# Kernel tuning notes

Hardware: AMD Instinct MI355X
Metric: run time of the kernel (lower is better)

## Reference

```python
import jax, jax.numpy as jnp
import numpy as np

NUM_HEADS = 16


def setup_inputs() -> dict:
    key = jax.random.key(0)
    k1, k2, k3 = jax.random.split(key, 3)
    T, B, E = 2048, 2, 1024
    x = jax.random.normal(k1, (T, B, E), dtype=jnp.float32)
    in_proj_w = jax.random.normal(k2, (E, 3 * E), dtype=jnp.float32) * (E ** -0.5)
    in_proj_b = jnp.zeros((3 * E,), dtype=jnp.float32)
    out_w = jax.random.normal(k3, (E, E), dtype=jnp.float32) * (E ** -0.5)
    out_b = jnp.zeros((E,), dtype=jnp.float32)
    return {"x": x, "in_proj_w": in_proj_w, "in_proj_b": in_proj_b,
            "out_w": out_w, "out_b": out_b}


def reference(x, in_proj_w, in_proj_b, out_w, out_b):
    # x: (tgt_len, bsz, embed_dim) -- seq-first, self-attention (q is k is v)
    T, B, E = x.shape
    H = NUM_HEADS
    D = E // H
    scaling = D ** -0.5
    # packed in-projection: einsum('bne,ef->bnf') over (T,B,E)
    proj = jnp.einsum('tbe,ef->tbf', x, in_proj_w) + in_proj_b
    q, k, v = jnp.split(proj, 3, axis=-1)  # each (T, B, E)
    # reshape to (T, B*H, D) then transpose to (B*H, T, D)
    q = q.reshape(T, B * H, D).transpose(1, 0, 2)
    k = k.reshape(T, B * H, D).transpose(1, 0, 2)
    v = v.reshape(T, B * H, D).transpose(1, 0, 2)
    # full O(T^2) attention matrix, scaling applied after QK^T as in source
    attn = jnp.einsum('bie,bje->bij', q, k) * scaling  # (B*H, T, T)
    attn = jax.nn.softmax(attn, axis=-1)
    out = jnp.einsum('bij,bje->bie', attn, v)  # (B*H, T, D)
    # faithful to source: reshape directly (no head transpose-back)
    out = out.reshape(B, T, E)
    out = jnp.einsum('bte,ef->btf', out, out_w) + out_b
    return out
```

## Files before the change

### kernel.cpp

```cpp
#include <hip/hip_runtime.h>
#include <stdint.h>

#define TSEQ 2048
#define NB 2
#define EMB 1024
#define NHEAD 16
#define HDIM 64
#define KSPLIT 4
#define NT (TSEQ / KSPLIT / 64)
#define QSCALE 0.18033688f

typedef __bf16 bf16x8 __attribute__((ext_vector_type(8)));
typedef __bf16 bf16x4 __attribute__((ext_vector_type(4)));
typedef float f32x4 __attribute__((ext_vector_type(4)));
typedef float f32x16 __attribute__((ext_vector_type(16)));
typedef unsigned int u32x4 __attribute__((ext_vector_type(4)));

__device__ __forceinline__ void gload_lds16(const void* g, void* lds) {
    __builtin_amdgcn_global_load_lds(
        (const __attribute__((address_space(1))) unsigned int*)g,
        (__attribute__((address_space(3))) unsigned int*)lds, 16, 0, 0);
}

__device__ __forceinline__ float fast_exp2(float x) {
#if __has_builtin(__builtin_amdgcn_exp2f)
    return __builtin_amdgcn_exp2f(x);
#else
    return exp2f(x);
#endif
}

__device__ __forceinline__ unsigned cvt_pk_bf16(float lo, float hi) {
    unsigned r;
    asm("v_cvt_pk_bf16_f32 %0, %1, %2" : "=v"(r) : "v"(lo), "v"(hi));
    return r;
}

__device__ __forceinline__ void swap32(unsigned& a, unsigned& b) {
    asm("v_permlane32_swap_b32 %0, %1" : "+v"(a), "+v"(b));
}

__device__ __forceinline__ bf16x8 as_bf16x8(u32x4 u) {
    union { u32x4 u; bf16x8 h; } c;
    c.u = u;
    return c.h;
}

__global__ __launch_bounds__(256) void cvt_x_kernel(
    const float* __restrict__ x, __bf16* __restrict__ xb)
{
    const size_t idx = ((size_t)blockIdx.x * 256 + threadIdx.x) * 4;
    float4 v = *(const float4*)(x + idx);
    bf16x4 o = { (__bf16)v.x, (__bf16)v.y, (__bf16)v.z, (__bf16)v.w };
    *(bf16x4*)(xb + idx) = o;
}

__global__ __launch_bounds__(256) void transpose_cvt_kernel(
    const float* __restrict__ w_in, const float* __restrict__ w_out,
    __bf16* __restrict__ wiT, __bf16* __restrict__ whT)
{
    __shared__ float tile[32][33];
    int bx = blockIdx.x;
    const int by = blockIdx.y;
    const float* src; __bf16* dst; int sn;
    if (bx < 96) { src = w_in;  dst = wiT; sn = 3072; }
    else         { bx -= 96; src = w_out; dst = whT; sn = 1024; }
    const int tx = threadIdx.x, ty = threadIdx.y;
    #pragma unroll
    for (int i = 0; i < 4; ++i)
        tile[ty + i * 8][tx] = src[(size_t)(by * 32 + ty + i * 8) * sn + bx * 32 + tx];
    __syncthreads();
    #pragma unroll
    for (int i = 0; i < 4; ++i) {
        float v = tile[tx][ty + i * 8];
        dst[(size_t)(bx * 32 + ty + i * 8) * 1024 + by * 32 + tx] = (__bf16)v;
    }
}

__global__ __launch_bounds__(256) void gemm_qkv_kernel(
    const __bf16* __restrict__ A, const __bf16* __restrict__ BT,
    const float* __restrict__ bias,
    __bf16* __restrict__ Oq, __bf16* __restrict__ Ok, __bf16* __restrict__ Ov)
{
    __shared__ __align__(16) __bf16 As[128 * 64];
    __shared__ __align__(16) __bf16 Bs[128 * 64];
    const int tid = threadIdx.x;
    const int wave = tid >> 6, lane = tid & 63;
    const int l16 = lane & 15, quad = lane >> 4;
    const int wm = wave >> 1, wn = wave & 1;
    const int m0 = blockIdx.y * 128, n0 = blockIdx.x * 128;

    f32x4 acc[4][4];
    #pragma unroll
    for (int mt = 0; mt < 4; ++mt)
        #pragma unroll
        for (int nt = 0; nt < 4; ++nt)
            #pragma unroll
            for (int r = 0; r < 4; ++r) acc[mt][nt][r] = 0.f;

    int smrow[4], schunk[4], sbase[4];
    #pragma unroll
    for (int i = 0; i < 4; ++i) {
        int linear = (wave * 4 + i) * 64 + lane;
        smrow[i] = linear >> 3;
        schunk[i] = (linear & 7) ^ (smrow[i] & 7);
        sbase[i] = (wave * 4 + i) * 512;
    }

    for (int k0 = 0; k0 < 1024; k0 += 64) {
        #pragma unroll
        for (int i = 0; i < 4; ++i) {
            gload_lds16(A + (size_t)(m0 + smrow[i]) * 1024 + k0 + schunk[i] * 8,
                        As + sbase[i]);
            gload_lds16(BT + (size_t)(n0 + smrow[i]) * 1024 + k0 + schunk[i] * 8,
                        Bs + sbase[i]);
        }
        __syncthreads();
        #pragma unroll
        for (int kk = 0; kk < 2; ++kk) {
            bf16x8 am[4], bn[4];
            #pragma unroll
            for (int mt = 0; mt < 4; ++mt) {
                int row = wm * 64 + mt * 16 + l16;
                int c = (kk * 4 + quad) ^ (row & 7);
                am[mt] = *(const bf16x8*)(As + row * 64 + c * 8);
            }
            #pragma unroll
            for (int nt = 0; nt < 4; ++nt) {
                int row = wn * 64 + nt * 16 + l16;
                int c = (kk * 4 + quad) ^ (row & 7);
                bn[nt] = *(const bf16x8*)(Bs + row * 64 + c * 8);
            }
            #pragma unroll
            for (int mt = 0; mt < 4; ++mt)
                #pragma unroll
                for (int nt = 0; nt < 4; ++nt)
                    acc[mt][nt] = __builtin_amdgcn_mfma_f32_16x16x32_bf16(
                        am[mt], bn[nt], acc[mt][nt], 0, 0, 0);
        }
        __syncthreads();
    }

    #pragma unroll
    for (int nt = 0; nt < 4; ++nt) {
        const int col = n0 + wn * 64 + nt * 16 + l16;
        const float bv = bias[col];
        const int sec = col >> 10, f = col & 1023;
        const int h = f >> 6, d = f & 63;
        #pragma unroll
        for (int mt = 0; mt < 4; ++mt)
            #pragma unroll
            for (int r = 0; r < 4; ++r) {
                const int row = m0 + wm * 64 + mt * 16 + quad * 4 + r;
                float v = acc[mt][nt][r] + bv;
                const int t = row >> 1, b = row & 1;
                const int bh = b * NHEAD + h;
                const size_t idx = ((size_t)bh * TSEQ + t) * HDIM + d;
                if (sec == 0)
                    Oq[idx] = (__bf16)(v * QSCALE);
                else if (sec == 1)
                    Ok[idx] = (__bf16)v;
                else
                    Ov[idx] = (__bf16)v;
            }
    }
}

__global__ __launch_bounds__(256) void vtrans_kernel(
    const __bf16* __restrict__ V, __bf16* __restrict__ Vt)
{
    __shared__ __bf16 T[64 * 67];
    const int bh = blockIdx.y;
    const int t0 = blockIdx.x * 64;
    const int tid = threadIdx.x;
    const int r = tid >> 2;
    const int c = (tid & 3) * 16;
    const __bf16* src = V + ((size_t)bh * TSEQ + t0 + r) * HDIM + c;
    bf16x8 a = *(const bf16x8*)src;
    bf16x8 b = *(const bf16x8*)(src + 8);
    #pragma unroll
    for (int j = 0; j < 8; ++j) {
        T[r * 67 + c + j] = a[j];
        T[r * 67 + c + 8 + j] = b[j];
    }
    __syncthreads();
    const int dr = tid >> 2;
    const int tc = (tid & 3) * 16;
    bf16x8 o0, o1;
    #pragma unroll
    for (int j = 0; j < 8; ++j) {
        o0[j] = T[(tc + j) * 67 + dr];
        o1[j] = T[(tc + 8 + j) * 67 + dr];
    }
    __bf16* dst = Vt + ((size_t)bh * HDIM + dr) * TSEQ + t0 + tc;
    *(bf16x8*)dst = o0;
    *(bf16x8*)(dst + 8) = o1;
}

__global__ __launch_bounds__(256, 4) void attn_mfma_kernel(
    const __bf16* __restrict__ Q, const __bf16* __restrict__ K,
    const __bf16* __restrict__ Vt,
    __bf16* __restrict__ O0, __bf16* __restrict__ O1,
    __bf16* __restrict__ O2, __bf16* __restrict__ O3,
    float* __restrict__ L0, float* __restrict__ L1,
    float* __restrict__ L2, float* __restrict__ L3)
{
    __shared__ __align__(16) __bf16 Ks[2][64 * 64];
    __shared__ __align__(16) __bf16 Vs[2][64 * 64];

    const int tid  = threadIdx.x;
    const int wave = tid >> 6;
    const int lane = tid & 63;
    const int l31  = lane & 31;
    const int hi   = lane >> 5;
    const int m7   = l31 & 7;

    const int lid = blockIdx.x;
    const int xcd = lid & 7;
    const int j   = lid >> 3;
    const int grp = xcd * 16 + (j >> 4);
    const int qb  = j & 15;
    const int bh  = grp >> 2;
    const int z   = grp & 3;

    const int q0   = qb * 128 + wave * 32;
    const int kbase0 = z * (TSEQ / KSPLIT);

    __bf16* __restrict__ Opart = (z == 0) ? O0 : (z == 1) ? O1 : (z == 2) ? O2 : O3;
    float*  __restrict__ Lpart = (z == 0) ? L0 : (z == 1) ? L1 : (z == 2) ? L2 : L3;

    bf16x8 qf[4];
    {
        const __bf16* Qrow = Q + ((size_t)bh * TSEQ + q0 + l31) * HDIM + 8 * hi;
        #pragma unroll
        for (int c = 0; c < 4; ++c)
            qf[c] = *(const bf16x8*)(Qrow + 16 * c);
    }

    f32x16 Oacc[2];
    #pragma unroll
    for (int dt = 0; dt < 2; ++dt)
        #pragma unroll
        for (int r = 0; r < 16; ++r) Oacc[dt][r] = 0.f;
    float l4[4] = {0.f, 0.f, 0.f, 0.f};

    const __bf16* Kbase = K + ((size_t)bh * TSEQ + kbase0) * HDIM;
    const __bf16* Vbase = Vt + (size_t)bh * HDIM * TSEQ + kbase0;

    int srow[2], schk[2];
    #pragma unroll
    for (int i = 0; i < 2; ++i) {
        const int s = wave * 2 + i;
        srow[i] = s * 8 + (lane >> 3);
        schk[i] = (lane & 7) ^ (srow[i] & 7);
    }

#define STAGE(buf, kt)                                                        \
    {                                                                         \
        _Pragma("unroll")                                                     \
        for (int i = 0; i < 2; ++i) {                                         \
            const int s = wave * 2 + i;                                       \
            gload_lds16(Kbase + (size_t)((kt) * 64 + srow[i]) * HDIM          \
                            + schk[i] * 8,                                    \
                        &Ks[buf][s * 512]);                                   \
            gload_lds16(Vbase + (size_t)srow[i] * TSEQ + (kt) * 64            \
                            + schk[i] * 8,                                    \
                        &Vs[buf][s * 512]);                                   \
        }                                                                     \
    }

    STAGE(0, 0);

    for (int kt = 0; kt < NT; ++kt) {
        const int b = kt & 1;
        __syncthreads();
        if (kt + 1 < NT) STAGE(b ^ 1, kt + 1);

        u32x4 pa[4];
        #pragma unroll
        for (int s = 0; s < 2; ++s) {
            f32x16 sacc;
            #pragma unroll
            for (int r = 0; r < 16; ++r) sacc[r] = 0.f;
            #pragma unroll
            for (int c = 0; c < 4; ++c) {
                bf16x8 kf = *(const bf16x8*)(
                    &Ks[b][(32 * s + l31) * 64 + (((c << 1) | hi) ^ m7) * 8]);
                sacc = __builtin_amdgcn_mfma_f32_32x32x16_bf16(
                    kf, qf[c], sacc, 0, 0, 0);
            }
            float p[16];
            #pragma unroll
            for (int r = 0; r < 16; ++r) {
                p[r] = fast_exp2(sacc[r]);
                l4[r & 3] += p[r];
            }
            unsigned x[8];
            #pragma unroll
            for (int i = 0; i < 8; ++i)
                x[i] = cvt_pk_bf16(p[2 * i], p[2 * i + 1]);
            swap32(x[0], x[2]); swap32(x[1], x[3]);
            swap32(x[4], x[6]); swap32(x[5], x[7]);
            pa[2 * s][0] = x[0]; pa[2 * s][1] = x[1];
            pa[2 * s][2] = x[2]; pa[2 * s][3] = x[3];
            pa[2 * s + 1][0] = x[4]; pa[2 * s + 1][1] = x[5];
            pa[2 * s + 1][2] = x[6]; pa[2 * s + 1][3] = x[7];
        }

        #pragma unroll
        for (int dt = 0; dt < 2; ++dt)
            #pragma unroll
            for (int ks = 0; ks < 4; ++ks) {
                bf16x8 vf = *(const bf16x8*)(
                    &Vs[b][(dt * 32 + l31) * 64 + (((ks << 1) | hi) ^ m7) * 8]);
                Oacc[dt] = __builtin_amdgcn_mfma_f32_32x32x16_bf16(
                    as_bf16x8(pa[ks]), vf, Oacc[dt], 0, 0, 0);
            }
    }
#undef STAGE

    {
        float v = (l4[0] + l4[1]) + (l4[2] + l4[3]);
        v += __shfl_xor(v, 32);
        if (hi == 0)
            Lpart[(size_t)bh * TSEQ + q0 + l31] = v;
    }

    const size_t base = ((size_t)bh * TSEQ + q0) * HDIM;
    #pragma unroll
    for (int dt = 0; dt < 2; ++dt)
        #pragma unroll
        for (int r = 0; r < 16; ++r) {
            const int q = (r & 3) + 8 * (r >> 2) + 4 * hi;
            Opart[base + (size_t)q * HDIM + dt * 32 + l31] =
                (__bf16)Oacc[dt][r];
        }
}

__global__ __launch_bounds__(256) void normalize_kernel(
    const __bf16* __restrict__ O0, const __bf16* __restrict__ O1,
    const __bf16* __restrict__ O2, const __bf16* __restrict__ O3,
    const float* __restrict__ L0, const float* __restrict__ L1,
    const float* __restrict__ L2, const float* __restrict__ L3,
    __bf16* __restrict__ Ob)
{
    const size_t gid = (size_t)blockIdx.x * 256 + threadIdx.x;
    const size_t idx = gid * 8;
    const size_t qi = idx >> 6;
    const float inv = 1.f / (L0[qi] + L1[qi] + L2[qi] + L3[qi]);
    bf16x8 a = *(const bf16x8*)(O0 + idx);
    bf16x8 b = *(const bf16x8*)(O1 + idx);
    bf16x8 c = *(const bf16x8*)(O2 + idx);
    bf16x8 d = *(const bf16x8*)(O3 + idx);
    bf16x8 o;
    #pragma unroll
    for (int j = 0; j < 8; ++j)
        o[j] = (__bf16)((((float)a[j] + (float)b[j]) +
                         ((float)c[j] + (float)d[j])) * inv);
    *(bf16x8*)(Ob + idx) = o;
}

__global__ __launch_bounds__(256) void gemm_out_kernel(
    const __bf16* __restrict__ A, const __bf16* __restrict__ BT,
    const float* __restrict__ bias, float* __restrict__ out)
{
    __shared__ __align__(16) __bf16 As[64 * 64];
    __shared__ __align__(16) __bf16 Bs[64 * 64];
    const int tid = threadIdx.x;
    const int wave = tid >> 6, lane = tid & 63;
    const int l16 = lane & 15, quad = lane >> 4;
    const int wm = wave >> 1, wn = wave & 1;
    const int m0 = blockIdx.y * 64, n0 = blockIdx.x * 64;

    f32x4 acc[2][2];
    #pragma unroll
    for (int mt = 0; mt < 2; ++mt)
        #pragma unroll
        for (int nt = 0; nt < 2; ++nt)
            #pragma unroll
            for (int r = 0; r < 4; ++r) acc[mt][nt][r] = 0.f;

    int srow[2], schk[2], sbase[2];
    #pragma unroll
    for (int i = 0; i < 2; ++i) {
        const int s = wave * 2 + i;
        srow[i] = s * 8 + (lane >> 3);
        schk[i] = (lane & 7) ^ (srow[i] & 7);
        sbase[i] = s * 512;
    }

    for (int k0 = 0; k0 < 1024; k0 += 64) {
        #pragma unroll
        for (int i = 0; i < 2; ++i) {
            gload_lds16(A + (size_t)(m0 + srow[i]) * 1024 + k0 + schk[i] * 8,
                        As + sbase[i]);
            gload_lds16(BT + (size_t)(n0 + srow[i]) * 1024 + k0 + schk[i] * 8,
                        Bs + sbase[i]);
        }
        __syncthreads();
        #pragma unroll
        for (int kk = 0; kk < 2; ++kk) {
            bf16x8 am[2], bn[2];
            #pragma unroll
            for (int mt = 0; mt < 2; ++mt) {
                int row = wm * 32 + mt * 16 + l16;
                int c = (kk * 4 + quad) ^ (row & 7);
                am[mt] = *(const bf16x8*)(As + row * 64 + c * 8);
            }
            #pragma unroll
            for (int nt = 0; nt < 2; ++nt) {
                int row = wn * 32 + nt * 16 + l16;
                int c = (kk * 4 + quad) ^ (row & 7);
                bn[nt] = *(const bf16x8*)(Bs + row * 64 + c * 8);
            }
            #pragma unroll
            for (int mt = 0; mt < 2; ++mt)
                #pragma unroll
                for (int nt = 0; nt < 2; ++nt)
                    acc[mt][nt] = __builtin_amdgcn_mfma_f32_16x16x32_bf16(
                        am[mt], bn[nt], acc[mt][nt], 0, 0, 0);
        }
        __syncthreads();
    }

    #pragma unroll
    for (int nt = 0; nt < 2; ++nt) {
        const int col = n0 + wn * 32 + nt * 16 + l16;
        const float bv = bias[col];
        #pragma unroll
        for (int mt = 0; mt < 2; ++mt)
            #pragma unroll
            for (int r = 0; r < 4; ++r) {
                const int row = m0 + wm * 32 + mt * 16 + quad * 4 + r;
                out[(size_t)row * 1024 + col] = acc[mt][nt][r] + bv;
            }
    }
}

extern "C" void kernel_launch(void* const* d_in, const int* in_sizes, int n_in,
                              void* d_out, int out_size, void* d_ws, size_t ws_size,
                              hipStream_t stream) {
    const float* x     = (const float*)d_in[0];
    const float* w_in  = (const float*)d_in[1];
    const float* b_in  = (const float*)d_in[2];
    const float* w_out = (const float*)d_in[3];
    const float* b_out = (const float*)d_in[4];
    float* out = (float*)d_out;

    const size_t M1 = (size_t)1024 * 1024;
    __bf16* ws  = (__bf16*)d_ws;
    __bf16* xb  = ws;
    __bf16* wiT = xb  + 4 * M1;
    __bf16* whT = wiT + 3 * M1;
    __bf16* Qb  = whT + 1 * M1;
    __bf16* Kb  = Qb  + 4 * M1;
    __bf16* Vt  = Kb  + 4 * M1;
    __bf16* O0  = Vt  + 4 * M1;
    __bf16* O1  = O0  + 4 * M1;
    float*  L0  = (float*)(O1 + 4 * M1);
    float*  L1  = L0 + 65536;
    float*  L2  = L1 + 65536;
    float*  L3  = L2 + 65536;
    __bf16* Vb  = (__bf16*)d_out;
    __bf16* O2  = (__bf16*)d_out;
    __bf16* O3  = O2 + 4 * M1;
    __bf16* Ob  = xb;

    cvt_x_kernel<<<4096, 256, 0, stream>>>(x, xb);
    transpose_cvt_kernel<<<dim3(128, 32), dim3(32, 8), 0, stream>>>(
        w_in, w_out, wiT, whT);
    gemm_qkv_kernel<<<dim3(24, 32), 256, 0, stream>>>(
        xb, wiT, b_in, Qb, Kb, Vb);
    vtrans_kernel<<<dim3(32, 32), 256, 0, stream>>>(Vb, Vt);
    attn_mfma_kernel<<<dim3(2048), 256, 0, stream>>>(
        Qb, Kb, Vt, O0, O1, O2, O3, L0, L1, L2, L3);
    normalize_kernel<<<2048, 256, 0, stream>>>(
        O0, O1, O2, O3, L0, L1, L2, L3, Ob);
    gemm_out_kernel<<<dim3(16, 64), 256, 0, stream>>>(
        Ob, whT, b_out, out);
}
```

Before: 199.2 us.

## Merge prep kernels, double query rows per attention wave, enlarge out-GEMM tiles

Three separate changes. The x conversion and weight transpose kernels become one launch, removing a launch. Each attention wave now handles 64 query rows in two groups that share each K/V fragment read from LDS, so the grid halves and occupancy is lowered to 2 blocks per CU. The output GEMM moves from 64x64 to 128x128 tiles with 4x4 MFMA accumulators per wave, raising reuse per loaded tile. The cost is higher register pressure and fewer blocks, which could reduce latency hiding.

```diff
diff --git a/kernel.cpp b/kernel.cpp
--- a/kernel.cpp
+++ b/kernel.cpp
@@ -46,26 +46,28 @@
     return c.h;
 }
 
-__global__ __launch_bounds__(256) void cvt_x_kernel(
-    const float* __restrict__ x, __bf16* __restrict__ xb)
-{
-    const size_t idx = ((size_t)blockIdx.x * 256 + threadIdx.x) * 4;
-    float4 v = *(const float4*)(x + idx);
-    bf16x4 o = { (__bf16)v.x, (__bf16)v.y, (__bf16)v.z, (__bf16)v.w };
-    *(bf16x4*)(xb + idx) = o;
-}
-
-__global__ __launch_bounds__(256) void transpose_cvt_kernel(
-    const float* __restrict__ w_in, const float* __restrict__ w_out,
-    __bf16* __restrict__ wiT, __bf16* __restrict__ whT)
+__global__ __launch_bounds__(256) void prep_kernel(
+    const float* __restrict__ x, const float* __restrict__ w_in,
+    const float* __restrict__ w_out,
+    __bf16* __restrict__ xb, __bf16* __restrict__ wiT, __bf16* __restrict__ whT)
 {
     __shared__ float tile[32][33];
-    int bx = blockIdx.x;
-    const int by = blockIdx.y;
+    int bid = blockIdx.x;
+    const int tid = threadIdx.x;
+    if (bid < 4096) {
+        const size_t idx = ((size_t)bid * 256 + tid) * 4;
+        float4 v = *(const float4*)(x + idx);
+        bf16x4 o = { (__bf16)v.x, (__bf16)v.y, (__bf16)v.z, (__bf16)v.w };
+        *(bf16x4*)(xb + idx) = o;
+        return;
+    }
+    bid -= 4096;
+    int bx = bid & 127;
+    const int by = bid >> 7;
     const float* src; __bf16* dst; int sn;
     if (bx < 96) { src = w_in;  dst = wiT; sn = 3072; }
     else         { bx -= 96; src = w_out; dst = whT; sn = 1024; }
-    const int tx = threadIdx.x, ty = threadIdx.y;
+    const int tx = tid & 31, ty = tid >> 5;
     #pragma unroll
     for (int i = 0; i < 4; ++i)
         tile[ty + i * 8][tx] = src[(size_t)(by * 32 + ty + i * 8) * sn + bx * 32 + tx];
@@ -197,7 +199,7 @@
     *(bf16x8*)(dst + 8) = o1;
 }
 
-__global__ __launch_bounds__(256, 4) void attn_mfma_kernel(
+__global__ __launch_bounds__(256, 2) void attn_mfma_kernel(
     const __bf16* __restrict__ Q, const __bf16* __restrict__ K,
     const __bf16* __restrict__ Vt,
     __bf16* __restrict__ O0, __bf16* __restrict__ O1,
@@ -218,31 +220,35 @@
     const int lid = blockIdx.x;
     const int xcd = lid & 7;
     const int j   = lid >> 3;
-    const int grp = xcd * 16 + (j >> 4);
-    const int qb  = j & 15;
+    const int grp = xcd * 16 + (j >> 3);
+    const int qb  = j & 7;
     const int bh  = grp >> 2;
     const int z   = grp & 3;
 
-    const int q0   = qb * 128 + wave * 32;
+    const int q0   = qb * 256 + wave * 64;
     const int kbase0 = z * (TSEQ / KSPLIT);
 
     __bf16* __restrict__ Opart = (z == 0) ? O0 : (z == 1) ? O1 : (z == 2) ? O2 : O3;
     float*  __restrict__ Lpart = (z == 0) ? L0 : (z == 1) ? L1 : (z == 2) ? L2 : L3;
 
-    bf16x8 qf[4];
-    {
-        const __bf16* Qrow = Q + ((size_t)bh * TSEQ + q0 + l31) * HDIM + 8 * hi;
+    bf16x8 qf[2][4];
+    #pragma unroll
+    for (int g = 0; g < 2; ++g) {
+        const __bf16* Qrow =
+            Q + ((size_t)bh * TSEQ + q0 + g * 32 + l31) * HDIM + 8 * hi;
         #pragma unroll
         for (int c = 0; c < 4; ++c)
-            qf[c] = *(const bf16x8*)(Qrow + 16 * c);
-    }
-
-    f32x16 Oacc[2];
-    #pragma unroll
-    for (int dt = 0; dt < 2; ++dt)
-        #pragma unroll
-        for (int r = 0; r < 16; ++r) Oacc[dt][r] = 0.f;
-    float l4[4] = {0.f, 0.f, 0.f, 0.f};
+            qf[g][c] = *(const bf16x8*)(Qrow + 16 * c);
+    }
+
+    f32x16 Oacc[2][2];
+    #pragma unroll
+    for (int g = 0; g < 2; ++g)
+        #pragma unroll
+        for (int dt = 0; dt < 2; ++dt)
+            #pragma unroll
+            for (int r = 0; r < 16; ++r) Oacc[g][dt][r] = 0.f;
+    float l4[2][4] = {{0.f, 0.f, 0.f, 0.f}, {0.f, 0.f, 0.f, 0.f}};
 
     const __bf16* Kbase = K + ((size_t)bh * TSEQ + kbase0) * HDIM;
     const __bf16* Vbase = Vt + (size_t)bh * HDIM * TSEQ + kbase0;
@@ -269,6 +275,26 @@
         }                                                                     \
     }
 
+#define SOFTMAX(sa, g, s)                                                     \
+    {                                                                         \
+        float p[16];                                                          \
+        _Pragma("unroll")                                                     \
+        for (int r = 0; r < 16; ++r) {                                        \
+            p[r] = fast_exp2((sa)[r]);                                        \
+            l4[g][r & 3] += p[r];                                             \
+        }                                                                     \
+        unsigned x[8];                                                        \
+        _Pragma("unroll")                                                     \
+        for (int i = 0; i < 8; ++i)                                           \
+            x[i] = cvt_pk_bf16(p[2 * i], p[2 * i + 1]);                       \
+        swap32(x[0], x[2]); swap32(x[1], x[3]);                               \
+        swap32(x[4], x[6]); swap32(x[5], x[7]);                               \
+        pa[g][2 * (s)][0] = x[0]; pa[g][2 * (s)][1] = x[1];                   \
+        pa[g][2 * (s)][2] = x[2]; pa[g][2 * (s)][3] = x[3];                   \
+        pa[g][2 * (s) + 1][0] = x[4]; pa[g][2 * (s) + 1][1] = x[5];           \
+        pa[g][2 * (s) + 1][2] = x[6]; pa[g][2 * (s) + 1][3] = x[7];           \
+    }
+
     STAGE(0, 0);
 
     for (int kt = 0; kt < NT; ++kt) {
@@ -276,35 +302,23 @@
         __syncthreads();
         if (kt + 1 < NT) STAGE(b ^ 1, kt + 1);
 
-        u32x4 pa[4];
+        u32x4 pa[2][4];
         #pragma unroll
         for (int s = 0; s < 2; ++s) {
-            f32x16 sacc;
-            #pragma unroll
-            for (int r = 0; r < 16; ++r) sacc[r] = 0.f;
+            f32x16 sa0, sa1;
+            #pragma unroll
+            for (int r = 0; r < 16; ++r) { sa0[r] = 0.f; sa1[r] = 0.f; }
             #pragma unroll
             for (int c = 0; c < 4; ++c) {
                 bf16x8 kf = *(const bf16x8*)(
                     &Ks[b][(32 * s + l31) * 64 + (((c << 1) | hi) ^ m7) * 8]);
-                sacc = __builtin_amdgcn_mfma_f32_32x32x16_bf16(
-                    kf, qf[c], sacc, 0, 0, 0);
-            }
-            float p[16];
-            #pragma unroll
-            for (int r = 0; r < 16; ++r) {
-                p[r] = fast_exp2(sacc[r]);
-                l4[r & 3] += p[r];
-            }
-            unsigned x[8];
-            #pragma unroll
-            for (int i = 0; i < 8; ++i)
-                x[i] = cvt_pk_bf16(p[2 * i], p[2 * i + 1]);
-            swap32(x[0], x[2]); swap32(x[1], x[3]);
-            swap32(x[4], x[6]); swap32(x[5], x[7]);
-            pa[2 * s][0] = x[0]; pa[2 * s][1] = x[1];
-            pa[2 * s][2] = x[2]; pa[2 * s][3] = x[3];
-            pa[2 * s + 1][0] = x[4]; pa[2 * s + 1][1] = x[5];
-            pa[2 * s + 1][2] = x[6]; pa[2 * s + 1][3] = x[7];
+                sa0 = __builtin_amdgcn_mfma_f32_32x32x16_bf16(
+                    kf, qf[0][c], sa0, 0, 0, 0);
+                sa1 = __builtin_amdgcn_mfma_f32_32x32x16_bf16(
+                    kf, qf[1][c], sa1, 0, 0, 0);
+            }
+            SOFTMAX(sa0, 0, s);
+            SOFTMAX(sa1, 1, s);
         }
 
         #pragma unroll
@@ -313,28 +327,34 @@
             for (int ks = 0; ks < 4; ++ks) {
                 bf16x8 vf = *(const bf16x8*)(
                     &Vs[b][(dt * 32 + l31) * 64 + (((ks << 1) | hi) ^ m7) * 8]);
-                Oacc[dt] = __builtin_amdgcn_mfma_f32_32x32x16_bf16(
-                    as_bf16x8(pa[ks]), vf, Oacc[dt], 0, 0, 0);
+                Oacc[0][dt] = __builtin_amdgcn_mfma_f32_32x32x16_bf16(
+                    as_bf16x8(pa[0][ks]), vf, Oacc[0][dt], 0, 0, 0);
+                Oacc[1][dt] = __builtin_amdgcn_mfma_f32_32x32x16_bf16(
+                    as_bf16x8(pa[1][ks]), vf, Oacc[1][dt], 0, 0, 0);
             }
     }
 #undef STAGE
-
-    {
-        float v = (l4[0] + l4[1]) + (l4[2] + l4[3]);
+#undef SOFTMAX
+
+    #pragma unroll
+    for (int g = 0; g < 2; ++g) {
+        float v = (l4[g][0] + l4[g][1]) + (l4[g][2] + l4[g][3]);
         v += __shfl_xor(v, 32);
         if (hi == 0)
-            Lpart[(size_t)bh * TSEQ + q0 + l31] = v;
+            Lpart[(size_t)bh * TSEQ + q0 + g * 32 + l31] = v;
     }
 
     const size_t base = ((size_t)bh * TSEQ + q0) * HDIM;
     #pragma unroll
-    for (int dt = 0; dt < 2; ++dt)
-        #pragma unroll
-        for (int r = 0; r < 16; ++r) {
-            const int q = (r & 3) + 8 * (r >> 2) + 4 * hi;
-            Opart[base + (size_t)q * HDIM + dt * 32 + l31] =
-                (__bf16)Oacc[dt][r];
-        }
+    for (int g = 0; g < 2; ++g)
+        #pragma unroll
+        for (int dt = 0; dt < 2; ++dt)
+            #pragma unroll
+            for (int r = 0; r < 16; ++r) {
+                const int q = g * 32 + (r & 3) + 8 * (r >> 2) + 4 * hi;
+                Opart[base + (size_t)q * HDIM + dt * 32 + l31] =
+                    (__bf16)Oacc[g][dt][r];
+            }
 }
 
 __global__ __launch_bounds__(256) void normalize_kernel(
@@ -364,59 +384,59 @@
     const __bf16* __restrict__ A, const __bf16* __restrict__ BT,
     const float* __restrict__ bias, float* __restrict__ out)
 {
-    __shared__ __align__(16) __bf16 As[64 * 64];
-    __shared__ __align__(16) __bf16 Bs[64 * 64];
+    __shared__ __align__(16) __bf16 As[128 * 64];
+    __shared__ __align__(16) __bf16 Bs[128 * 64];
     const int tid = threadIdx.x;
     const int wave = tid >> 6, lane = tid & 63;
     const int l16 = lane & 15, quad = lane >> 4;
     const int wm = wave >> 1, wn = wave & 1;
-    const int m0 = blockIdx.y * 64, n0 = blockIdx.x * 64;
-
-    f32x4 acc[2][2];
-    #pragma unroll
-    for (int mt = 0; mt < 2; ++mt)
-        #pragma unroll
-        for (int nt = 0; nt < 2; ++nt)
+    const int m0 = blockIdx.y * 128, n0 = blockIdx.x * 128;
+
+    f32x4 acc[4][4];
+    #pragma unroll
+    for (int mt = 0; mt < 4; ++mt)
+        #pragma unroll
+        for (int nt = 0; nt < 4; ++nt)
             #pragma unroll
             for (int r = 0; r < 4; ++r) acc[mt][nt][r] = 0.f;
 
-    int srow[2], schk[2], sbase[2];
-    #pragma unroll
-    for (int i = 0; i < 2; ++i) {
-        const int s = wave * 2 + i;
-        srow[i] = s * 8 + (lane >> 3);
-        schk[i] = (lane & 7) ^ (srow[i] & 7);
-        sbase[i] = s * 512;
+    int smrow[4], schunk[4], sbase[4];
+    #pragma unroll
+    for (int i = 0; i < 4; ++i) {
+        int linear = (wave * 4 + i) * 64 + lane;
+        smrow[i] = linear >> 3;
+        schunk[i] = (linear & 7) ^ (smrow[i] & 7);
+        sbase[i] = (wave * 4 + i) * 512;
     }
 
     for (int k0 = 0; k0 < 1024; k0 += 64) {
         #pragma unroll
-        for (int i = 0; i < 2; ++i) {
-            gload_lds16(A + (size_t)(m0 + srow[i]) * 1024 + k0 + schk[i] * 8,
+        for (int i = 0; i < 4; ++i) {
+            gload_lds16(A + (size_t)(m0 + smrow[i]) * 1024 + k0 + schunk[i] * 8,
                         As + sbase[i]);
-            gload_lds16(BT + (size_t)(n0 + srow[i]) * 1024 + k0 + schk[i] * 8,
+            gload_lds16(BT + (size_t)(n0 + smrow[i]) * 1024 + k0 + schunk[i] * 8,
                         Bs + sbase[i]);
         }
         __syncthreads();
         #pragma unroll
         for (int kk = 0; kk < 2; ++kk) {
-            bf16x8 am[2], bn[2];
-            #pragma unroll
-            for (int mt = 0; mt < 2; ++mt) {
-                int row = wm * 32 + mt * 16 + l16;
+            bf16x8 am[4], bn[4];
+            #pragma unroll
+            for (int mt = 0; mt < 4; ++mt) {
+                int row = wm * 64 + mt * 16 + l16;
                 int c = (kk * 4 + quad) ^ (row & 7);
                 am[mt] = *(const bf16x8*)(As + row * 64 + c * 8);
             }
             #pragma unroll
-            for (int nt = 0; nt < 2; ++nt) {
-                int row = wn * 32 + nt * 16 + l16;
+            for (int nt = 0; nt < 4; ++nt) {
+                int row = wn * 64 + nt * 16 + l16;
                 int c = (kk * 4 + quad) ^ (row & 7);
                 bn[nt] = *(const bf16x8*)(Bs + row * 64 + c * 8);
             }
             #pragma unroll
-            for (int mt = 0; mt < 2; ++mt)
+            for (int mt = 0; mt < 4; ++mt)
                 #pragma unroll
-                for (int nt = 0; nt < 2; ++nt)
+                for (int nt = 0; nt < 4; ++nt)
                     acc[mt][nt] = __builtin_amdgcn_mfma_f32_16x16x32_bf16(
                         am[mt], bn[nt], acc[mt][nt], 0, 0, 0);
         }
@@ -424,14 +444,14 @@
     }
 
     #pragma unroll
-    for (int nt = 0; nt < 2; ++nt) {
-        const int col = n0 + wn * 32 + nt * 16 + l16;
+    for (int nt = 0; nt < 4; ++nt) {
+        const int col = n0 + wn * 64 + nt * 16 + l16;
         const float bv = bias[col];
         #pragma unroll
-        for (int mt = 0; mt < 2; ++mt)
+        for (int mt = 0; mt < 4; ++mt)
             #pragma unroll
             for (int r = 0; r < 4; ++r) {
-                const int row = m0 + wm * 32 + mt * 16 + quad * 4 + r;
+                const int row = m0 + wm * 64 + mt * 16 + quad * 4 + r;
                 out[(size_t)row * 1024 + col] = acc[mt][nt][r] + bv;
             }
     }
@@ -466,16 +486,14 @@
     __bf16* O3  = O2 + 4 * M1;
     __bf16* Ob  = xb;
 
-    cvt_x_kernel<<<4096, 256, 0, stream>>>(x, xb);
-    transpose_cvt_kernel<<<dim3(128, 32), dim3(32, 8), 0, stream>>>(
-        w_in, w_out, wiT, whT);
+    prep_kernel<<<8192, 256, 0, stream>>>(x, w_in, w_out, xb, wiT, whT);
     gemm_qkv_kernel<<<dim3(24, 32), 256, 0, stream>>>(
         xb, wiT, b_in, Qb, Kb, Vb);
     vtrans_kernel<<<dim3(32, 32), 256, 0, stream>>>(Vb, Vt);
-    attn_mfma_kernel<<<dim3(2048), 256, 0, stream>>>(
+    attn_mfma_kernel<<<dim3(1024), 256, 0, stream>>>(
         Qb, Kb, Vt, O0, O1, O2, O3, L0, L1, L2, L3);
     normalize_kernel<<<2048, 256, 0, stream>>>(
         O0, O1, O2, O3, L0, L1, L2, L3, Ob);
-    gemm_out_kernel<<<dim3(16, 64), 256, 0, stream>>>(
+    gemm_out_kernel<<<dim3(8, 32), 256, 0, stream>>>(
         Ob, whT, b_out, out);
 }
```

New measurement: 200.9 us. About the same (+0.9%).
